# Optimization experiments

Measured on AMD Instinct MI355X. Metric: run time of the kernel, lower is better.

The kernel has to match this reference:

```python
import jax, jax.numpy as jnp
import numpy as np

B, S, H, DK, DV, D = 1024, 8, 16, 32, 32, 512


def setup_inputs() -> dict:
    key = jax.random.key(0)
    ks = jax.random.split(key, 12)
    s = 1.0 / np.sqrt(D)
    return {
        "Q": jax.random.normal(ks[0], (B, S, D), jnp.float32),
        "K": jax.random.normal(ks[1], (B, S, D), jnp.float32),
        "V": jax.random.normal(ks[2], (B, S, D), jnp.float32),
        "attn_mask": jax.random.bernoulli(ks[3], 0.2, (B, S, S)),
        "hyper": jax.random.normal(ks[4], (B, H * S * DK), jnp.float32),
        "Wq": jax.random.normal(ks[5], (H * DK, D), jnp.float32) * s,
        "bq": jnp.zeros((H * DK,), jnp.float32),
        "Wk": jax.random.normal(ks[6], (H * DK, D), jnp.float32) * s,
        "bk": jnp.zeros((H * DK,), jnp.float32),
        "Wv": jax.random.normal(ks[7], (H * DV, D), jnp.float32) * s,
        "bv": jnp.zeros((H * DV,), jnp.float32),
        "Wo": jax.random.normal(ks[8], (D, H * DV), jnp.float32) * s,
        "bo": jnp.zeros((D,), jnp.float32),
        "ln_g": jnp.ones((D,), jnp.float32),
        "ln_b": jnp.zeros((D,), jnp.float32),
    }


def reference(Q, K, V, attn_mask, hyper, Wq, bq, Wk, bk, Wv, bv, Wo, bo, ln_g, ln_b):
    # QKV projections -> [B, H, S, dk]
    q = (Q @ Wq.T + bq).reshape(B, S, H, DK).transpose(0, 2, 1, 3)
    k = (K @ Wk.T + bk).reshape(B, S, H, DK).transpose(0, 2, 1, 3)
    v = (V @ Wv.T + bv).reshape(B, S, H, DV).transpose(0, 2, 1, 3)
    # scaled dot-product attention with mask
    scores = jnp.einsum('bhqd,bhkd->bhqk', q, k) / np.sqrt(DK).astype(np.float32)
    scores = jnp.where(attn_mask[:, None, :, :], -1e9, scores)
    weights = jax.nn.softmax(scores, axis=-1)
    # hyper-gated AV
    context = jnp.einsum('bhqk,bhkd->bhqd', weights, v) * hyper.reshape(B, H, S, DK)
    context = context.transpose(0, 2, 1, 3).reshape(B, S, H * DV)
    # output projection + residual layernorm (eps=1e-5)
    out = context @ Wo.T + bo + Q
    mu = out.mean(axis=-1, keepdims=True)
    var = out.var(axis=-1, keepdims=True)
    out = (out - mu) * jax.lax.rsqrt(var + 1e-5) * ln_g + ln_b
    return (out, weights)
```

## Files before the change

### kernel.cpp

```cpp
#include <hip/hip_runtime.h>
#include <hip/hip_bf16.h>
#include <cstdint>

#define NB 1024
#define ND 512
#define NM 8192

typedef __attribute__((ext_vector_type(8))) short short8;
typedef __attribute__((ext_vector_type(8))) __bf16 bf16x8;
typedef __attribute__((ext_vector_type(4))) float f32x4;
typedef __attribute__((ext_vector_type(4))) unsigned short ushort4v;

__device__ __forceinline__ unsigned short f2bf(float f) {
  uint32_t x = __builtin_bit_cast(uint32_t, f);
  x += 0x7fffu + ((x >> 16) & 1u);
  return (unsigned short)(x >> 16);
}
__device__ __forceinline__ float bf2f(unsigned short u) {
  return __builtin_bit_cast(float, (uint32_t)u << 16);
}
__device__ __forceinline__ f32x4 mfma16(short8 a, short8 b, f32x4 c) {
  return __builtin_amdgcn_mfma_f32_16x16x32_bf16(
      __builtin_bit_cast(bf16x8, a), __builtin_bit_cast(bf16x8, b), c, 0, 0, 0);
}

__global__ __launch_bounds__(256) void convert_w(
    const float* __restrict__ Wq, const float* __restrict__ Wk,
    const float* __restrict__ Wv, const float* __restrict__ Wo,
    unsigned short* __restrict__ Wqb, unsigned short* __restrict__ Wkb,
    unsigned short* __restrict__ Wvb, unsigned short* __restrict__ Wob) {
  const int idx = blockIdx.x * 256 + threadIdx.x;
  const int sel = idx >> 15, o = (idx & 32767) * 8;
  const float* src = sel == 0 ? Wq : sel == 1 ? Wk : sel == 2 ? Wv : Wo;
  unsigned short* dst = sel == 0 ? Wqb : sel == 1 ? Wkb : sel == 2 ? Wvb : Wob;
  const float4 a = ((const float4*)(src + o))[0];
  const float4 b = ((const float4*)(src + o))[1];
  short8 r;
  r[0] = (short)f2bf(a.x); r[1] = (short)f2bf(a.y);
  r[2] = (short)f2bf(a.z); r[3] = (short)f2bf(a.w);
  r[4] = (short)f2bf(b.x); r[5] = (short)f2bf(b.y);
  r[6] = (short)f2bf(b.z); r[7] = (short)f2bf(b.w);
  *(short8*)(dst + o) = r;
}

template <bool A_F32, int MODE>
__device__ __forceinline__ void gemm_tile(const void* __restrict__ A,
                                          const unsigned short* __restrict__ W,
                                          const float* __restrict__ bias,
                                          const float* __restrict__ resid,
                                          void* __restrict__ C, int mBase, int nBase) {
  __shared__ unsigned short As[128 * 64];
  __shared__ unsigned short Bs[128 * 64];
  const int tid = threadIdx.x;
  const int lane = tid & 63, wid = tid >> 6;
  const int wm = wid >> 2, wn = wid & 3;
  const int l15 = lane & 15, l4 = lane >> 4;
  f32x4 acc[4][2] = {};

  for (int kt = 0; kt < 8; ++kt) {
    const int kBase = kt * 64;
#pragma unroll
    for (int i = 0; i < 2; ++i) {
      const int Lb = i * 8192 + tid * 16;
      const int r = Lb >> 7;
      const int ce = (Lb & 127) >> 1;
      const int P = Lb ^ ((r & 7) << 4);
      short8 av;
      if (A_F32) {
        const float* src = (const float*)A + (size_t)(mBase + r) * ND + kBase + ce;
        const float4 a = ((const float4*)src)[0];
        const float4 b = ((const float4*)src)[1];
        av[0] = (short)f2bf(a.x); av[1] = (short)f2bf(a.y);
        av[2] = (short)f2bf(a.z); av[3] = (short)f2bf(a.w);
        av[4] = (short)f2bf(b.x); av[5] = (short)f2bf(b.y);
        av[6] = (short)f2bf(b.z); av[7] = (short)f2bf(b.w);
      } else {
        av = *(const short8*)((const unsigned short*)A +
                              (size_t)(mBase + r) * ND + kBase + ce);
      }
      const short8 wv = *(const short8*)(W + (size_t)(nBase + r) * ND + kBase + ce);
      *(short8*)((char*)As + P) = av;
      *(short8*)((char*)Bs + P) = wv;
    }
    __syncthreads();
#pragma unroll
    for (int kk = 0; kk < 2; ++kk) {
      short8 af[4], bf4[2];
#pragma unroll
      for (int m = 0; m < 4; ++m) {
        const int r = wm * 64 + m * 16 + l15;
        const int Lb = r * 128 + kk * 64 + l4 * 16;
        af[m] = *(const short8*)((char*)As + (Lb ^ ((r & 7) << 4)));
      }
#pragma unroll
      for (int n = 0; n < 2; ++n) {
        const int r = wn * 32 + n * 16 + l15;
        const int Lb = r * 128 + kk * 64 + l4 * 16;
        bf4[n] = *(const short8*)((char*)Bs + (Lb ^ ((r & 7) << 4)));
      }
#pragma unroll
      for (int m = 0; m < 4; ++m)
#pragma unroll
        for (int n = 0; n < 2; ++n)
          acc[m][n] = mfma16(af[m], bf4[n], acc[m][n]);
    }
    __syncthreads();
  }

#pragma unroll
  for (int m = 0; m < 4; ++m)
#pragma unroll
    for (int n = 0; n < 2; ++n) {
      const int gn = nBase + wn * 32 + n * 16 + l15;
      const float bb = bias ? bias[gn] : 0.f;
#pragma unroll
      for (int r4 = 0; r4 < 4; ++r4) {
        const int gm = mBase + wm * 64 + m * 16 + l4 * 4 + r4;
        float val = acc[m][n][r4] + bb;
        if (MODE == 0) {
          ((unsigned short*)C)[(size_t)gm * ND + gn] = f2bf(val);
        } else {
          val += resid[(size_t)gm * ND + gn];
          ((float*)C)[(size_t)gm * ND + gn] = val;
        }
      }
    }
}

__global__ __launch_bounds__(512) void gemm_qkv(
    const float* __restrict__ Q, const float* __restrict__ K,
    const float* __restrict__ V, const unsigned short* __restrict__ Wqb,
    const unsigned short* __restrict__ Wkb, const unsigned short* __restrict__ Wvb,
    const float* __restrict__ bq, const float* __restrict__ bk,
    const float* __restrict__ bv, unsigned short* __restrict__ qo,
    unsigned short* __restrict__ ko, unsigned short* __restrict__ vo) {
  const int bid = blockIdx.x;
  const int lid = (bid & 7) * 96 + (bid >> 3);
  const int by = lid / 12, bx = lid % 12;
  const int seg = bx >> 2, nloc = bx & 3;
  const float* A = seg == 0 ? Q : seg == 1 ? K : V;
  const unsigned short* W = seg == 0 ? Wqb : seg == 1 ? Wkb : Wvb;
  const float* bias = seg == 0 ? bq : seg == 1 ? bk : bv;
  unsigned short* C = seg == 0 ? qo : seg == 1 ? ko : vo;
  gemm_tile<true, 0>(A, W, bias, nullptr, C, by * 128, nloc * 128);
}

__global__ __launch_bounds__(512) void gemm_wo(const unsigned short* __restrict__ ctx,
                                               const unsigned short* __restrict__ Wob,
                                               const float* __restrict__ bo,
                                               const float* __restrict__ Qres,
                                               float* __restrict__ out) {
  const int bid = blockIdx.x;
  const int lid = (bid & 7) * 32 + (bid >> 3);
  const int by = lid >> 2, bx = lid & 3;
  gemm_tile<false, 1>(ctx, Wob, bo, Qres, out, by * 128, bx * 128);
}

__global__ __launch_bounds__(256) void attn_kernel(
    const unsigned short* __restrict__ q, const unsigned short* __restrict__ k,
    const unsigned short* __restrict__ v, const int* __restrict__ mask,
    const float* __restrict__ hyper, float* __restrict__ wout,
    unsigned short* __restrict__ ctx) {
  const int tid = threadIdx.x;
  const int wid = tid >> 6, lane = tid & 63;
  const int t = blockIdx.x * 4 + wid;
  const int b = t >> 4, h = t & 15;
  const int i = lane >> 3, j = lane & 7;

  const unsigned short* qrow = q + (size_t)(b * 8 + i) * ND + h * 32;
  const unsigned short* krow = k + (size_t)(b * 8 + j) * ND + h * 32;
  float dot = 0.f;
#pragma unroll
  for (int c = 0; c < 4; ++c) {
    const short8 qv = ((const short8*)qrow)[c];
    const short8 kv = ((const short8*)krow)[c];
#pragma unroll
    for (int e = 0; e < 8; ++e)
      dot += bf2f((unsigned short)qv[e]) * bf2f((unsigned short)kv[e]);
  }
  float score = dot * 0.17677669529663687f;
  if (mask[b * 64 + i * 8 + j]) score = -1e9f;

  float mx = score;
#pragma unroll
  for (int o = 4; o; o >>= 1) mx = fmaxf(mx, __shfl_xor(mx, o, 8));
  const float e = __expf(score - mx);
  float sm = e;
#pragma unroll
  for (int o = 4; o; o >>= 1) sm += __shfl_xor(sm, o, 8);
  const float w = e / sm;
  wout[(size_t)t * 64 + lane] = w;

  const int d0 = (lane & 7) * 4;
  float c0 = 0, c1 = 0, c2 = 0, c3 = 0;
#pragma unroll
  for (int jj = 0; jj < 8; ++jj) {
    const float wj = __shfl(w, jj, 8);
    const ushort4v vv = *(const ushort4v*)(v + (size_t)(b * 8 + jj) * ND + h * 32 + d0);
    c0 += wj * bf2f(vv[0]); c1 += wj * bf2f(vv[1]);
    c2 += wj * bf2f(vv[2]); c3 += wj * bf2f(vv[3]);
  }
  const float4 hv = *(const float4*)(hyper + (size_t)b * 4096 + h * 256 + i * 32 + d0);
  ushort4v co;
  co[0] = f2bf(c0 * hv.x); co[1] = f2bf(c1 * hv.y);
  co[2] = f2bf(c2 * hv.z); co[3] = f2bf(c3 * hv.w);
  *(ushort4v*)(ctx + (size_t)(b * 8 + i) * ND + h * 32 + d0) = co;
}

__global__ __launch_bounds__(256) void ln_kernel(float* __restrict__ io,
                                                 const float* __restrict__ g,
                                                 const float* __restrict__ be) {
  const int tid = threadIdx.x, wid = tid >> 6, lane = tid & 63;
  const size_t row = (size_t)blockIdx.x * 4 + wid;
  float* prow = io + row * ND + lane * 8;
  float4 x0 = ((float4*)prow)[0], x1 = ((float4*)prow)[1];
  float s = x0.x + x0.y + x0.z + x0.w + x1.x + x1.y + x1.z + x1.w;
  float sq = x0.x * x0.x + x0.y * x0.y + x0.z * x0.z + x0.w * x0.w +
             x1.x * x1.x + x1.y * x1.y + x1.z * x1.z + x1.w * x1.w;
#pragma unroll
  for (int o = 32; o; o >>= 1) {
    s += __shfl_xor(s, o, 64);
    sq += __shfl_xor(sq, o, 64);
  }
  const float mu = s * (1.f / 512.f);
  const float inv = rsqrtf(sq * (1.f / 512.f) - mu * mu + 1e-5f);
  const float4 g0 = ((const float4*)(g + lane * 8))[0];
  const float4 g1 = ((const float4*)(g + lane * 8))[1];
  const float4 e0 = ((const float4*)(be + lane * 8))[0];
  const float4 e1 = ((const float4*)(be + lane * 8))[1];
  float4 o0, o1;
  o0.x = (x0.x - mu) * inv * g0.x + e0.x; o0.y = (x0.y - mu) * inv * g0.y + e0.y;
  o0.z = (x0.z - mu) * inv * g0.z + e0.z; o0.w = (x0.w - mu) * inv * g0.w + e0.w;
  o1.x = (x1.x - mu) * inv * g1.x + e1.x; o1.y = (x1.y - mu) * inv * g1.y + e1.y;
  o1.z = (x1.z - mu) * inv * g1.z + e1.z; o1.w = (x1.w - mu) * inv * g1.w + e1.w;
  ((float4*)prow)[0] = o0;
  ((float4*)prow)[1] = o1;
}

extern "C" void kernel_launch(void* const* d_in, const int* in_sizes, int n_in,
                              void* d_out, int out_size, void* d_ws, size_t ws_size,
                              hipStream_t stream) {
  const float* Q = (const float*)d_in[0];
  const float* K = (const float*)d_in[1];
  const float* V = (const float*)d_in[2];
  const int* msk = (const int*)d_in[3];
  const float* hyper = (const float*)d_in[4];
  const float* Wq = (const float*)d_in[5];
  const float* bq = (const float*)d_in[6];
  const float* Wk = (const float*)d_in[7];
  const float* bk = (const float*)d_in[8];
  const float* Wv = (const float*)d_in[9];
  const float* bv = (const float*)d_in[10];
  const float* Wo = (const float*)d_in[11];
  const float* bo = (const float*)d_in[12];
  const float* lg = (const float*)d_in[13];
  const float* lb = (const float*)d_in[14];

  float* out = (float*)d_out;
  float* wout = out + (size_t)NM * ND;

  const size_t MAT = (size_t)NM * ND;
  unsigned short* qb = (unsigned short*)d_ws;
  unsigned short* kb = qb + MAT;
  unsigned short* vb = kb + MAT;
  unsigned short* ctxb = vb + MAT;
  unsigned short* Wqb = ctxb + MAT;
  unsigned short* Wkb = Wqb + (size_t)ND * ND;
  unsigned short* Wvb = Wkb + (size_t)ND * ND;
  unsigned short* Wob = Wvb + (size_t)ND * ND;

  convert_w<<<512, 256, 0, stream>>>(Wq, Wk, Wv, Wo, Wqb, Wkb, Wvb, Wob);
  gemm_qkv<<<768, 512, 0, stream>>>(Q, K, V, Wqb, Wkb, Wvb,
                                    bq, bk, bv, qb, kb, vb);
  attn_kernel<<<4096, 256, 0, stream>>>(qb, kb, vb, msk, hyper, wout, ctxb);
  gemm_wo<<<256, 512, 0, stream>>>(ctxb, Wob, bo, Q, out);
  ln_kernel<<<2048, 256, 0, stream>>>(out, lg, lb);
}
```

Baseline: 74.64 us.

## Fuse QKV projection, attention, output projection and layernorm into one kernel

Replaces the four kernels (QKV GEMM, attention, Wo GEMM, layernorm) with a single persistent-style kernel. Each 512-thread block owns 32 rows (4 batches), keeps q/k/v and the context in swizzled LDS, and streams weight tiles through double-buffered LDS using global_load_lds with manual vmcnt waits. This removes the bf16 q/k/v/ctx round trips to global memory and the extra launches. The cost is only 256 blocks with large LDS use, which limits occupancy and leaves the tall-skinny GEMMs with little parallelism per CU.

```diff
diff --git a/kernel.cpp b/kernel.cpp
--- a/kernel.cpp
+++ b/kernel.cpp
@@ -23,6 +23,23 @@
   return __builtin_amdgcn_mfma_f32_16x16x32_bf16(
       __builtin_bit_cast(bf16x8, a), __builtin_bit_cast(bf16x8, b), c, 0, 0, 0);
 }
+__device__ __forceinline__ void gl_lds16(const unsigned short* g, unsigned short* lds) {
+  __builtin_amdgcn_global_load_lds(
+      (const __attribute__((address_space(1))) unsigned int*)g,
+      (__attribute__((address_space(3))) unsigned int*)lds, 16, 0, 0);
+}
+__device__ __forceinline__ short8 cvt8(float4 a, float4 b) {
+  short8 r;
+  r[0] = (short)f2bf(a.x); r[1] = (short)f2bf(a.y);
+  r[2] = (short)f2bf(a.z); r[3] = (short)f2bf(a.w);
+  r[4] = (short)f2bf(b.x); r[5] = (short)f2bf(b.y);
+  r[6] = (short)f2bf(b.z); r[7] = (short)f2bf(b.w);
+  return r;
+}
+#define VMCNT0() asm volatile("s_waitcnt vmcnt(0)" ::: "memory")
+#define VMCNT4() asm volatile("s_waitcnt vmcnt(4)" ::: "memory")
+#define LGKMCNT0() asm volatile("s_waitcnt lgkmcnt(0)" ::: "memory")
+#define BAR() __builtin_amdgcn_s_barrier()
 
 __global__ __launch_bounds__(256) void convert_w(
     const float* __restrict__ Wq, const float* __restrict__ Wk,
@@ -35,206 +52,261 @@
   unsigned short* dst = sel == 0 ? Wqb : sel == 1 ? Wkb : sel == 2 ? Wvb : Wob;
   const float4 a = ((const float4*)(src + o))[0];
   const float4 b = ((const float4*)(src + o))[1];
-  short8 r;
-  r[0] = (short)f2bf(a.x); r[1] = (short)f2bf(a.y);
-  r[2] = (short)f2bf(a.z); r[3] = (short)f2bf(a.w);
-  r[4] = (short)f2bf(b.x); r[5] = (short)f2bf(b.y);
-  r[6] = (short)f2bf(b.z); r[7] = (short)f2bf(b.w);
-  *(short8*)(dst + o) = r;
-}
-
-template <bool A_F32, int MODE>
-__device__ __forceinline__ void gemm_tile(const void* __restrict__ A,
-                                          const unsigned short* __restrict__ W,
-                                          const float* __restrict__ bias,
-                                          const float* __restrict__ resid,
-                                          void* __restrict__ C, int mBase, int nBase) {
-  __shared__ unsigned short As[128 * 64];
-  __shared__ unsigned short Bs[128 * 64];
+  *(short8*)(dst + o) = cvt8(a, b);
+}
+
+__global__ __launch_bounds__(512, 2) void fused_kernel(
+    const float* __restrict__ Qf, const float* __restrict__ Kf,
+    const float* __restrict__ Vf, const int* __restrict__ mask,
+    const float* __restrict__ hyper,
+    const unsigned short* __restrict__ Wqb, const unsigned short* __restrict__ Wkb,
+    const unsigned short* __restrict__ Wvb, const unsigned short* __restrict__ Wob,
+    const float* __restrict__ bq, const float* __restrict__ bk,
+    const float* __restrict__ bv, const float* __restrict__ bo,
+    const float* __restrict__ lg, const float* __restrict__ lb,
+    float* __restrict__ out, float* __restrict__ wout) {
+  __shared__ unsigned short Wt0[512 * 32];
+  __shared__ unsigned short Wt1[512 * 32];
+  __shared__ unsigned short qs[32 * 512];
+  __shared__ unsigned short ks[32 * 512];
+  __shared__ unsigned short vs[32 * 512];
+
   const int tid = threadIdx.x;
   const int lane = tid & 63, wid = tid >> 6;
-  const int wm = wid >> 2, wn = wid & 3;
   const int l15 = lane & 15, l4 = lane >> 4;
-  f32x4 acc[4][2] = {};
-
-  for (int kt = 0; kt < 8; ++kt) {
-    const int kBase = kt * 64;
-#pragma unroll
-    for (int i = 0; i < 2; ++i) {
-      const int Lb = i * 8192 + tid * 16;
-      const int r = Lb >> 7;
-      const int ce = (Lb & 127) >> 1;
-      const int P = Lb ^ ((r & 7) << 4);
-      short8 av;
-      if (A_F32) {
-        const float* src = (const float*)A + (size_t)(mBase + r) * ND + kBase + ce;
-        const float4 a = ((const float4*)src)[0];
-        const float4 b = ((const float4*)src)[1];
-        av[0] = (short)f2bf(a.x); av[1] = (short)f2bf(a.y);
-        av[2] = (short)f2bf(a.z); av[3] = (short)f2bf(a.w);
-        av[4] = (short)f2bf(b.x); av[5] = (short)f2bf(b.y);
-        av[6] = (short)f2bf(b.z); av[7] = (short)f2bf(b.w);
-      } else {
-        av = *(const short8*)((const unsigned short*)A +
-                              (size_t)(mBase + r) * ND + kBase + ce);
+  const int b0 = blockIdx.x;
+  const int mBase = b0 * 32;
+
+  f32x4 acc[2][4] = {};
+
+  auto stageW = [&](const unsigned short* W, int ktl, unsigned short* wt) {
+#pragma unroll
+    for (int i = 0; i < 4; ++i) {
+      const int rp = wid * 32 + i * 8 + (lane >> 3);
+      const int gl = (lane & 7) ^ (rp & 7);
+      const int rsrc = rp * 2 + (gl >> 2);
+      const int cel = ktl * 32 + (gl & 3) * 8;
+      gl_lds16(W + (size_t)rsrc * 512 + cel, wt + (wid * 64 + i * 16) * 32);
+    }
+  };
+  auto computeG = [&](const unsigned short* wt, short8 a0, short8 a1) {
+    short8 bfr[4];
+#pragma unroll
+    for (int nf = 0; nf < 4; ++nf) {
+      const int n = wid * 64 + nf * 16 + l15;
+      const int rp = n >> 1;
+      const int gp = ((n & 1) * 4 + l4) ^ (rp & 7);
+      bfr[nf] = *(const short8*)((const char*)wt + rp * 128 + gp * 16);
+    }
+#pragma unroll
+    for (int nf = 0; nf < 4; ++nf) {
+      acc[0][nf] = mfma16(a0, bfr[nf], acc[0][nf]);
+      acc[1][nf] = mfma16(a1, bfr[nf], acc[1][nf]);
+    }
+  };
+  auto issueA = [&](int ktg, float4 (&d)[4]) {
+    if (ktg >= 48) return;
+    const float* Am = ktg < 16 ? Qf : (ktg < 32 ? Kf : Vf);
+    const int ktl = ktg & 15;
+#pragma unroll
+    for (int m = 0; m < 2; ++m) {
+      const float* p = Am + (size_t)(mBase + m * 16 + l15) * 512 + ktl * 32 + l4 * 8;
+      d[m * 2] = ((const float4*)p)[0];
+      d[m * 2 + 1] = ((const float4*)p)[1];
+    }
+  };
+  auto epiQKV = [&](unsigned short* dst, const float* bias) {
+#pragma unroll
+    for (int nf = 0; nf < 4; ++nf) {
+      const int col = wid * 64 + nf * 16 + l15;
+      const float bb = bias[col];
+      const int g = col >> 3;
+      const int eb = (col & 7) * 2;
+#pragma unroll
+      for (int m = 0; m < 2; ++m)
+#pragma unroll
+        for (int r = 0; r < 4; ++r) {
+          const int row = m * 16 + l4 * 4 + r;
+          *(unsigned short*)((char*)dst + row * 1024 + ((g ^ (row & 7)) * 16) + eb) =
+              f2bf(acc[m][nf][r] + bb);
+          acc[m][nf][r] = 0.f;
+        }
+    }
+  };
+
+  float4 aP0[4], aP1[4];
+  short8 afr0, afr1;
+  stageW(Wqb, 0, Wt0);
+  issueA(0, aP0);
+  issueA(1, aP1);
+  VMCNT0();
+  afr0 = cvt8(aP0[0], aP0[1]);
+  afr1 = cvt8(aP0[2], aP0[3]);
+  BAR();
+  for (int kt2 = 0; kt2 < 48; kt2 += 2) {
+    const int kB = kt2 + 1;
+    const unsigned short* WB = kB < 16 ? Wqb : (kB < 32 ? Wkb : Wvb);
+    if (kB < 48) stageW(WB, kB & 15, Wt1);
+    issueA(kt2 + 2, aP0);
+    computeG(Wt0, afr0, afr1);
+    VMCNT4();
+    afr0 = cvt8(aP1[0], aP1[1]);
+    afr1 = cvt8(aP1[2], aP1[3]);
+    BAR();
+    if (kB + 1 < 48) {
+      const unsigned short* WC = (kB + 1) < 16 ? Wqb : ((kB + 1) < 32 ? Wkb : Wvb);
+      stageW(WC, (kB + 1) & 15, Wt0);
+    }
+    issueA(kB + 2, aP1);
+    if (kt2 == 46) VMCNT0();
+    computeG(Wt1, afr0, afr1);
+    if (kB == 15) epiQKV(qs, bq);
+    else if (kB == 31) epiQKV(ks, bk);
+    else if (kB == 47) epiQKV(vs, bv);
+    VMCNT4();
+    afr0 = cvt8(aP0[0], aP0[1]);
+    afr1 = cvt8(aP0[2], aP0[3]);
+    BAR();
+  }
+
+  const int ai = lane >> 3, aj = lane & 7;
+  for (int p = 0; p < 8; ++p) {
+    const int bb = p >> 1, hh = p & 1;
+    const int h = wid * 2 + hh;
+    const int b = b0 * 4 + bb;
+    const int qrow = bb * 8 + ai, krow = bb * 8 + aj;
+    float dot = 0.f;
+#pragma unroll
+    for (int c = 0; c < 4; ++c) {
+      const short8 qv = *(const short8*)((const char*)qs + qrow * 1024 +
+                                         (((h * 4 + c) ^ (qrow & 7)) * 16));
+      const short8 kv = *(const short8*)((const char*)ks + krow * 1024 +
+                                         (((h * 4 + c) ^ (krow & 7)) * 16));
+#pragma unroll
+      for (int e = 0; e < 8; ++e)
+        dot += bf2f((unsigned short)qv[e]) * bf2f((unsigned short)kv[e]);
+    }
+    float score = dot * 0.17677669529663687f;
+    if (mask[b * 64 + ai * 8 + aj]) score = -1e9f;
+    float mx = score;
+#pragma unroll
+    for (int o = 4; o; o >>= 1) mx = fmaxf(mx, __shfl_xor(mx, o, 8));
+    const float e = __expf(score - mx);
+    float sm = e;
+#pragma unroll
+    for (int o = 4; o; o >>= 1) sm += __shfl_xor(sm, o, 8);
+    const float w = e / sm;
+    wout[(size_t)(b * 16 + h) * 64 + lane] = w;
+    const int d0 = (lane & 7) * 4;
+    const int gv = h * 4 + ((lane & 7) >> 1);
+    const int ob = (lane & 1) * 8;
+    float c0 = 0, c1 = 0, c2 = 0, c3 = 0;
+#pragma unroll
+    for (int jj = 0; jj < 8; ++jj) {
+      const float wj = __shfl(w, jj, 8);
+      const int vrow = bb * 8 + jj;
+      const ushort4v vv = *(const ushort4v*)((const char*)vs + vrow * 1024 +
+                                             ((gv ^ (vrow & 7)) * 16) + ob);
+      c0 += wj * bf2f(vv[0]); c1 += wj * bf2f(vv[1]);
+      c2 += wj * bf2f(vv[2]); c3 += wj * bf2f(vv[3]);
+    }
+    const float4 hv = *(const float4*)(hyper + (size_t)b * 4096 + h * 256 + ai * 32 + d0);
+    ushort4v co;
+    co[0] = f2bf(c0 * hv.x); co[1] = f2bf(c1 * hv.y);
+    co[2] = f2bf(c2 * hv.z); co[3] = f2bf(c3 * hv.w);
+    *(ushort4v*)((char*)qs + qrow * 1024 + ((gv ^ (qrow & 7)) * 16) + ob) = co;
+  }
+
+  auto ldCtx = [&](int kt, short8& a0, short8& a1) {
+#pragma unroll
+    for (int m = 0; m < 2; ++m) {
+      const int row = m * 16 + l15;
+      const int g = kt * 4 + l4;
+      const short8 v = *(const short8*)((const char*)qs + row * 1024 +
+                                        ((g ^ (row & 7)) * 16));
+      if (m == 0) a0 = v; else a1 = v;
+    }
+  };
+  stageW(Wob, 0, Wt0);
+  LGKMCNT0();
+  VMCNT0();
+  BAR();
+  for (int kt = 0; kt < 16; kt += 2) {
+    if (kt + 1 < 16) stageW(Wob, kt + 1, Wt1);
+    ldCtx(kt, afr0, afr1);
+    computeG(Wt0, afr0, afr1);
+    VMCNT0();
+    BAR();
+    if (kt + 2 < 16) stageW(Wob, kt + 2, Wt0);
+    ldCtx(kt + 1, afr0, afr1);
+    computeG(Wt1, afr0, afr1);
+    VMCNT0();
+    BAR();
+  }
+
+  float bov[4], lgv[4], lbv[4];
+#pragma unroll
+  for (int nf = 0; nf < 4; ++nf) {
+    const int col = wid * 64 + nf * 16 + l15;
+    bov[nf] = bo[col]; lgv[nf] = lg[col]; lbv[nf] = lb[col];
+  }
+  float ps[8], ps2[8];
+#pragma unroll
+  for (int m = 0; m < 2; ++m)
+#pragma unroll
+    for (int r = 0; r < 4; ++r) {
+      const int row = m * 16 + l4 * 4 + r;
+      float s = 0.f, s2 = 0.f;
+#pragma unroll
+      for (int nf = 0; nf < 4; ++nf) {
+        const int col = wid * 64 + nf * 16 + l15;
+        float v = acc[m][nf][r] + bov[nf] + Qf[(size_t)(mBase + row) * 512 + col];
+        acc[m][nf][r] = v;
+        s += v; s2 += v * v;
       }
-      const short8 wv = *(const short8*)(W + (size_t)(nBase + r) * ND + kBase + ce);
-      *(short8*)((char*)As + P) = av;
-      *(short8*)((char*)Bs + P) = wv;
-    }
-    __syncthreads();
-#pragma unroll
-    for (int kk = 0; kk < 2; ++kk) {
-      short8 af[4], bf4[2];
-#pragma unroll
-      for (int m = 0; m < 4; ++m) {
-        const int r = wm * 64 + m * 16 + l15;
-        const int Lb = r * 128 + kk * 64 + l4 * 16;
-        af[m] = *(const short8*)((char*)As + (Lb ^ ((r & 7) << 4)));
+      ps[m * 4 + r] = s; ps2[m * 4 + r] = s2;
+    }
+#pragma unroll
+  for (int idx = 0; idx < 8; ++idx)
+#pragma unroll
+    for (int o = 1; o < 16; o <<= 1) {
+      ps[idx] += __shfl_xor(ps[idx], o, 64);
+      ps2[idx] += __shfl_xor(ps2[idx], o, 64);
+    }
+  float* scr = (float*)ks;
+  float* scr2 = scr + 256;
+  if (l15 == 0) {
+#pragma unroll
+    for (int m = 0; m < 2; ++m)
+#pragma unroll
+      for (int r = 0; r < 4; ++r) {
+        const int row = m * 16 + l4 * 4 + r;
+        scr[row * 8 + wid] = ps[m * 4 + r];
+        scr2[row * 8 + wid] = ps2[m * 4 + r];
       }
-#pragma unroll
-      for (int n = 0; n < 2; ++n) {
-        const int r = wn * 32 + n * 16 + l15;
-        const int Lb = r * 128 + kk * 64 + l4 * 16;
-        bf4[n] = *(const short8*)((char*)Bs + (Lb ^ ((r & 7) << 4)));
+  }
+  LGKMCNT0();
+  BAR();
+#pragma unroll
+  for (int m = 0; m < 2; ++m)
+#pragma unroll
+    for (int r = 0; r < 4; ++r) {
+      const int row = m * 16 + l4 * 4 + r;
+      float s = 0.f, s2 = 0.f;
+#pragma unroll
+      for (int wv = 0; wv < 8; ++wv) {
+        s += scr[row * 8 + wv];
+        s2 += scr2[row * 8 + wv];
       }
-#pragma unroll
-      for (int m = 0; m < 4; ++m)
-#pragma unroll
-        for (int n = 0; n < 2; ++n)
-          acc[m][n] = mfma16(af[m], bf4[n], acc[m][n]);
-    }
-    __syncthreads();
-  }
-
-#pragma unroll
-  for (int m = 0; m < 4; ++m)
-#pragma unroll
-    for (int n = 0; n < 2; ++n) {
-      const int gn = nBase + wn * 32 + n * 16 + l15;
-      const float bb = bias ? bias[gn] : 0.f;
-#pragma unroll
-      for (int r4 = 0; r4 < 4; ++r4) {
-        const int gm = mBase + wm * 64 + m * 16 + l4 * 4 + r4;
-        float val = acc[m][n][r4] + bb;
-        if (MODE == 0) {
-          ((unsigned short*)C)[(size_t)gm * ND + gn] = f2bf(val);
-        } else {
-          val += resid[(size_t)gm * ND + gn];
-          ((float*)C)[(size_t)gm * ND + gn] = val;
-        }
+      const float mu = s * (1.f / 512.f);
+      const float inv = rsqrtf(s2 * (1.f / 512.f) - mu * mu + 1e-5f);
+#pragma unroll
+      for (int nf = 0; nf < 4; ++nf) {
+        const int col = wid * 64 + nf * 16 + l15;
+        out[(size_t)(mBase + row) * 512 + col] =
+            (acc[m][nf][r] - mu) * inv * lgv[nf] + lbv[nf];
       }
     }
-}
-
-__global__ __launch_bounds__(512) void gemm_qkv(
-    const float* __restrict__ Q, const float* __restrict__ K,
-    const float* __restrict__ V, const unsigned short* __restrict__ Wqb,
-    const unsigned short* __restrict__ Wkb, const unsigned short* __restrict__ Wvb,
-    const float* __restrict__ bq, const float* __restrict__ bk,
-    const float* __restrict__ bv, unsigned short* __restrict__ qo,
-    unsigned short* __restrict__ ko, unsigned short* __restrict__ vo) {
-  const int bid = blockIdx.x;
-  const int lid = (bid & 7) * 96 + (bid >> 3);
-  const int by = lid / 12, bx = lid % 12;
-  const int seg = bx >> 2, nloc = bx & 3;
-  const float* A = seg == 0 ? Q : seg == 1 ? K : V;
-  const unsigned short* W = seg == 0 ? Wqb : seg == 1 ? Wkb : Wvb;
-  const float* bias = seg == 0 ? bq : seg == 1 ? bk : bv;
-  unsigned short* C = seg == 0 ? qo : seg == 1 ? ko : vo;
-  gemm_tile<true, 0>(A, W, bias, nullptr, C, by * 128, nloc * 128);
-}
-
-__global__ __launch_bounds__(512) void gemm_wo(const unsigned short* __restrict__ ctx,
-                                               const unsigned short* __restrict__ Wob,
-                                               const float* __restrict__ bo,
-                                               const float* __restrict__ Qres,
-                                               float* __restrict__ out) {
-  const int bid = blockIdx.x;
-  const int lid = (bid & 7) * 32 + (bid >> 3);
-  const int by = lid >> 2, bx = lid & 3;
-  gemm_tile<false, 1>(ctx, Wob, bo, Qres, out, by * 128, bx * 128);
-}
-
-__global__ __launch_bounds__(256) void attn_kernel(
-    const unsigned short* __restrict__ q, const unsigned short* __restrict__ k,
-    const unsigned short* __restrict__ v, const int* __restrict__ mask,
-    const float* __restrict__ hyper, float* __restrict__ wout,
-    unsigned short* __restrict__ ctx) {
-  const int tid = threadIdx.x;
-  const int wid = tid >> 6, lane = tid & 63;
-  const int t = blockIdx.x * 4 + wid;
-  const int b = t >> 4, h = t & 15;
-  const int i = lane >> 3, j = lane & 7;
-
-  const unsigned short* qrow = q + (size_t)(b * 8 + i) * ND + h * 32;
-  const unsigned short* krow = k + (size_t)(b * 8 + j) * ND + h * 32;
-  float dot = 0.f;
-#pragma unroll
-  for (int c = 0; c < 4; ++c) {
-    const short8 qv = ((const short8*)qrow)[c];
-    const short8 kv = ((const short8*)krow)[c];
-#pragma unroll
-    for (int e = 0; e < 8; ++e)
-      dot += bf2f((unsigned short)qv[e]) * bf2f((unsigned short)kv[e]);
-  }
-  float score = dot * 0.17677669529663687f;
-  if (mask[b * 64 + i * 8 + j]) score = -1e9f;
-
-  float mx = score;
-#pragma unroll
-  for (int o = 4; o; o >>= 1) mx = fmaxf(mx, __shfl_xor(mx, o, 8));
-  const float e = __expf(score - mx);
-  float sm = e;
-#pragma unroll
-  for (int o = 4; o; o >>= 1) sm += __shfl_xor(sm, o, 8);
-  const float w = e / sm;
-  wout[(size_t)t * 64 + lane] = w;
-
-  const int d0 = (lane & 7) * 4;
-  float c0 = 0, c1 = 0, c2 = 0, c3 = 0;
-#pragma unroll
-  for (int jj = 0; jj < 8; ++jj) {
-    const float wj = __shfl(w, jj, 8);
-    const ushort4v vv = *(const ushort4v*)(v + (size_t)(b * 8 + jj) * ND + h * 32 + d0);
-    c0 += wj * bf2f(vv[0]); c1 += wj * bf2f(vv[1]);
-    c2 += wj * bf2f(vv[2]); c3 += wj * bf2f(vv[3]);
-  }
-  const float4 hv = *(const float4*)(hyper + (size_t)b * 4096 + h * 256 + i * 32 + d0);
-  ushort4v co;
-  co[0] = f2bf(c0 * hv.x); co[1] = f2bf(c1 * hv.y);
-  co[2] = f2bf(c2 * hv.z); co[3] = f2bf(c3 * hv.w);
-  *(ushort4v*)(ctx + (size_t)(b * 8 + i) * ND + h * 32 + d0) = co;
-}
-
-__global__ __launch_bounds__(256) void ln_kernel(float* __restrict__ io,
-                                                 const float* __restrict__ g,
-                                                 const float* __restrict__ be) {
-  const int tid = threadIdx.x, wid = tid >> 6, lane = tid & 63;
-  const size_t row = (size_t)blockIdx.x * 4 + wid;
-  float* prow = io + row * ND + lane * 8;
-  float4 x0 = ((float4*)prow)[0], x1 = ((float4*)prow)[1];
-  float s = x0.x + x0.y + x0.z + x0.w + x1.x + x1.y + x1.z + x1.w;
-  float sq = x0.x * x0.x + x0.y * x0.y + x0.z * x0.z + x0.w * x0.w +
-             x1.x * x1.x + x1.y * x1.y + x1.z * x1.z + x1.w * x1.w;
-#pragma unroll
-  for (int o = 32; o; o >>= 1) {
-    s += __shfl_xor(s, o, 64);
-    sq += __shfl_xor(sq, o, 64);
-  }
-  const float mu = s * (1.f / 512.f);
-  const float inv = rsqrtf(sq * (1.f / 512.f) - mu * mu + 1e-5f);
-  const float4 g0 = ((const float4*)(g + lane * 8))[0];
-  const float4 g1 = ((const float4*)(g + lane * 8))[1];
-  const float4 e0 = ((const float4*)(be + lane * 8))[0];
-  const float4 e1 = ((const float4*)(be + lane * 8))[1];
-  float4 o0, o1;
-  o0.x = (x0.x - mu) * inv * g0.x + e0.x; o0.y = (x0.y - mu) * inv * g0.y + e0.y;
-  o0.z = (x0.z - mu) * inv * g0.z + e0.z; o0.w = (x0.w - mu) * inv * g0.w + e0.w;
-  o1.x = (x1.x - mu) * inv * g1.x + e1.x; o1.y = (x1.y - mu) * inv * g1.y + e1.y;
-  o1.z = (x1.z - mu) * inv * g1.z + e1.z; o1.w = (x1.w - mu) * inv * g1.w + e1.w;
-  ((float4*)prow)[0] = o0;
-  ((float4*)prow)[1] = o1;
 }
 
 extern "C" void kernel_launch(void* const* d_in, const int* in_sizes, int n_in,
@@ -259,20 +331,12 @@
   float* out = (float*)d_out;
   float* wout = out + (size_t)NM * ND;
 
-  const size_t MAT = (size_t)NM * ND;
-  unsigned short* qb = (unsigned short*)d_ws;
-  unsigned short* kb = qb + MAT;
-  unsigned short* vb = kb + MAT;
-  unsigned short* ctxb = vb + MAT;
-  unsigned short* Wqb = ctxb + MAT;
+  unsigned short* Wqb = (unsigned short*)d_ws;
   unsigned short* Wkb = Wqb + (size_t)ND * ND;
   unsigned short* Wvb = Wkb + (size_t)ND * ND;
   unsigned short* Wob = Wvb + (size_t)ND * ND;
 
   convert_w<<<512, 256, 0, stream>>>(Wq, Wk, Wv, Wo, Wqb, Wkb, Wvb, Wob);
-  gemm_qkv<<<768, 512, 0, stream>>>(Q, K, V, Wqb, Wkb, Wvb,
-                                    bq, bk, bv, qb, kb, vb);
-  attn_kernel<<<4096, 256, 0, stream>>>(qb, kb, vb, msk, hyper, wout, ctxb);
-  gemm_wo<<<256, 512, 0, stream>>>(ctxb, Wob, bo, Q, out);
-  ln_kernel<<<2048, 256, 0, stream>>>(out, lg, lb);
-}
+  fused_kernel<<<256, 512, 0, stream>>>(Q, K, V, msk, hyper, Wqb, Wkb, Wvb, Wob,
+                                        bq, bk, bv, bo, lg, lb, out, wout);
+}
```

Result: slower. 112.3 us (+50.5%).
